# Kernel tuning notes

Hardware: AMD Instinct MI355X
Metric: run time of the kernel (lower is better)

Reference implementation:

```python
import jax, jax.numpy as jnp
import numpy as np

T_PRED = 30   # max_pred_time * hz
B = 2048      # number of trajectory segments (batch)
D = 256       # n_hidden_after_deconv
DH = 128      # n_hidden_after_deconv / 2


def setup_inputs() -> dict:
    key = jax.random.key(0)
    k1, k2, k3, k4 = jax.random.split(key, 4)
    return {
        "encode_samples": jax.random.normal(k1, (T_PRED, B, D), dtype=jnp.float32),
        "representation_cur": jax.random.normal(k2, (B, DH), dtype=jnp.float32),
        "Wk_w": jax.random.normal(k3, (T_PRED, D, DH), dtype=jnp.float32) * (1.0 / np.sqrt(DH)),
        "Wk_b": jax.random.normal(k4, (T_PRED, D), dtype=jnp.float32) * 0.01,
    }


def reference(encode_samples, representation_cur, Wk_w, Wk_b):
    # encode_samples: [T, B, D] future encoder outputs (c_{t+i})
    # Wk_w: [T, D, DH] per-step Linear weights (torch layout [out,in]); Wk_b: [T, D]
    T, Bn, Dd = encode_samples.shape
    # pred[i] = Wk[i](representation_cur)  -> [T, B, D]
    pred = jnp.einsum('bh,tdh->tbd', representation_cur, Wk_w) + Wk_b[:, None, :]
    # total_i = encode_samples[i] @ pred[i].T  -> [T, B, B]
    totals = jnp.einsum('tbd,tcd->tbc', encode_samples, pred)
    # nce += sum(diag(log_softmax(total, dim=1))) per step (torch LogSoftmax default dim=1 on 2D)
    logp = jax.nn.log_softmax(totals, axis=2)
    nce = jnp.sum(jnp.diagonal(logp, axis1=1, axis2=2))
    calc_step = Bn * T  # all pred_steps > T-1 (all segments long enough)
    nce = nce / (-1.0 * calc_step)
    # accuracy from the LAST step (matches the original loop-carried `correct`/`batch_idx`)
    probs = jax.nn.softmax(totals[-1], axis=1)          # softmax over dim=1
    correct = jnp.sum(jnp.argmax(probs, axis=0) == jnp.arange(Bn))  # argmax over dim=0
    accuracy = correct.astype(jnp.float32) / Bn
    return (accuracy, nce, jnp.asarray(Bn), jnp.asarray(calc_step))
```

## Files before the change

kernel.cpp:

```cpp
#include <hip/hip_runtime.h>
#include <math.h>

typedef unsigned short u16;
typedef unsigned int   u32;
typedef unsigned long long u64;

#define T_PRED 30
#define BN 2048
#define DD 256
#define DHH 128
#define ESHIFT 64.0f

typedef __attribute__((ext_vector_type(8))) short short8;
typedef __attribute__((ext_vector_type(4))) float f32x4;

#define WS_S      4096
#define WS_TABLE  (WS_S + 245760)
#define WS_ZEND   (WS_TABLE + 16384)
#define WS_WH     WS_ZEND
#define WS_WL     (WS_WH + 1966080)
#define WS_RH     (WS_WL + 1966080)
#define WS_RL     (WS_RH + 524288)
#define WS_GH     (WS_RL + 524288)
#define WS_GL29   (WS_GH + 15728640)
#define WS_T29    (WS_GL29 + 524288)

__device__ __forceinline__ u16 bf16_rne(float f) {
    u32 u = __float_as_uint(f);
    u32 r = u + 0x7fffu + ((u >> 16) & 1u);
    return (u16)(r >> 16);
}

__device__ __forceinline__ short8 pack_hi8(const float* f) {
    short8 r;
#pragma unroll
    for (int k = 0; k < 8; ++k) r[k] = (short)(u16)(__float_as_uint(f[k]) >> 16);
    return r;
}
__device__ __forceinline__ short8 pack_lo8(const float* f) {
    short8 r;
#pragma unroll
    for (int k = 0; k < 8; ++k) {
        float hf = __uint_as_float(__float_as_uint(f[k]) & 0xffff0000u);
        r[k] = (short)bf16_rne(f[k] - hf);
    }
    return r;
}

#define AS1 __attribute__((address_space(1)))
#define AS3 __attribute__((address_space(3)))

__global__ __launch_bounds__(256) void prep_kernel(
    const float* __restrict__ rep, const float* __restrict__ Ww,
    u16* __restrict__ Rh, u16* __restrict__ Rl,
    u16* __restrict__ Wh, u16* __restrict__ Wl, u32* __restrict__ wsz)
{
    const int bx = blockIdx.x, tid = threadIdx.x;
    for (int i = bx * 256 + tid; i < 66560; i += 32768) wsz[i] = 0;

    if (bx < 120) {
        __shared__ float tile[64][132];
        const int t = bx >> 2, d0 = (bx & 3) * 64;
        for (int it = 0; it < 8; ++it) {
            int idx = tid + it * 256;
            int row = idx >> 5, off = (idx & 31) * 4;
            *(float4*)&tile[row][off] =
                *(const float4*)&Ww[((size_t)t * DD + d0 + row) * DHH + off];
        }
        __syncthreads();
        const int h = tid >> 1, half = tid & 1;
        const bool lo = (t == T_PRED - 1);
        for (int d4 = 0; d4 < 32; d4 += 4) {
            ushort4 hv, lv;
            u16* hp = (u16*)&hv; u16* lp = (u16*)&lv;
#pragma unroll
            for (int k = 0; k < 4; ++k) {
                float v = tile[half * 32 + d4 + k][h];
                u16 hb = bf16_rne(v);
                hp[k] = hb;
                float hf = __uint_as_float((u32)hb << 16);
                lp[k] = bf16_rne(v - hf);
            }
            size_t o = (size_t)t * DHH * DD + (size_t)h * DD + d0 + half * 32 + d4;
            *(ushort4*)&Wh[o] = hv;
            if (lo) *(ushort4*)&Wl[o] = lv;
        }
    } else {
        int base = (bx - 120) * 256 + tid;
        for (int p = 0; p < 32; ++p) {
            int i = base + p * 2048;
            float4 v = ((const float4*)rep)[i];
            float vv[4] = {v.x, v.y, v.z, v.w};
            u16 h[4], l[4];
#pragma unroll
            for (int k = 0; k < 4; ++k) {
                h[k] = bf16_rne(vv[k]);
                float hf = __uint_as_float((u32)h[k] << 16);
                l[k] = bf16_rne(vv[k] - hf);
            }
            ((ushort4*)Rh)[i] = make_ushort4(h[0], h[1], h[2], h[3]);
            ((ushort4*)Rl)[i] = make_ushort4(l[0], l[1], l[2], l[3]);
        }
    }
}

__global__ __launch_bounds__(256) void g_fused_kernel(
    const float* __restrict__ E, const u16* __restrict__ Wh,
    const u16* __restrict__ Wl, u16* __restrict__ Gh,
    u16* __restrict__ Gh29, u16* __restrict__ Gl29)
{
    __shared__ __attribute__((aligned(16))) u32 esm[2][4096];
    __shared__ __attribute__((aligned(16))) u16 wsm[2][4096];
    const int y    = blockIdx.y;
    const int tid  = threadIdx.x;
    const int lane = tid & 63;
    const int w    = tid >> 6;
    const int ml   = lane & 15;
    const int quad = lane >> 4;

    if (y < 29) {
        const int t    = y;
        const int row0 = blockIdx.x * 128;
        const int wr   = (w >> 1) * 64;
        const int wc   = (w & 1) * 64;
        const float* Et = E + (size_t)t * BN * DD;
        const u16*   Wt = Wh + (size_t)t * DHH * DD;
        const int erow_l = lane >> 3, eunit = lane & 7;
        const int wcol_l = lane >> 2, wunit = lane & 3;

        auto stage = [&](int buf, int kc) {
#pragma unroll
            for (int n = 0; n < 4; ++n) {
                int q = w * 4 + n;
                int row = q * 8 + erow_l;
                int unit = (eunit - row) & 7;
                const float* g = Et + (size_t)(row0 + row) * DD + kc * 32 + unit * 4;
                __builtin_amdgcn_global_load_lds((const AS1 u32*)g,
                    (AS3 u32*)(&esm[buf][q * 256]), 16, 0, 0);
            }
#pragma unroll
            for (int n = 0; n < 2; ++n) {
                int q = w * 2 + n;
                int col = q * 16 + wcol_l;
                int unit = (wunit - col) & 3;
                const u16* g = Wt + (size_t)col * DD + kc * 32 + unit * 8;
                __builtin_amdgcn_global_load_lds((const AS1 u32*)g,
                    (AS3 u32*)(&wsm[buf][q * 512]), 16, 0, 0);
            }
        };

        f32x4 acc[4][4];
#pragma unroll
        for (int i = 0; i < 4; ++i)
#pragma unroll
            for (int j = 0; j < 4; ++j) acc[i][j] = (f32x4){0.f, 0.f, 0.f, 0.f};

        stage(0, 0);
        __syncthreads();
#pragma unroll 1
        for (int kc = 0; kc < 8; ++kc) {
            if (kc < 7) stage((kc + 1) & 1, kc + 1);
            const int pb = kc & 1;
            short8 ah[4], bh[4];
#pragma unroll
            for (int i = 0; i < 4; ++i) {
                int row = wr + i * 16 + ml;
                float4 f0 = *(const float4*)&esm[pb][row * 32 + (((quad * 2 + 0 + row) & 7) * 4)];
                float4 f1 = *(const float4*)&esm[pb][row * 32 + (((quad * 2 + 1 + row) & 7) * 4)];
                float f[8] = {f0.x, f0.y, f0.z, f0.w, f1.x, f1.y, f1.z, f1.w};
                ah[i] = pack_hi8(f);
            }
#pragma unroll
            for (int j = 0; j < 4; ++j) {
                int col = wc + j * 16 + ml;
                bh[j] = *(const short8*)&wsm[pb][col * 32 + ((quad + col) & 3) * 8];
            }
#pragma unroll
            for (int i = 0; i < 4; ++i)
#pragma unroll
                for (int j = 0; j < 4; ++j)
                    acc[i][j] = __builtin_amdgcn_mfma_f32_16x16x32_bf16(ah[i], bh[j], acc[i][j], 0, 0, 0);
            __syncthreads();
        }

#pragma unroll
        for (int i = 0; i < 4; ++i)
#pragma unroll
            for (int j = 0; j < 4; ++j)
#pragma unroll
                for (int r = 0; r < 4; ++r) {
                    int row = row0 + wr + i * 16 + quad * 4 + r;
                    int col = wc + j * 16 + ml;
                    Gh[((size_t)t * BN + row) * DHH + col] = bf16_rne(acc[i][j][r]);
                }
    } else {
        const int row0 = ((y - 29) * 16 + blockIdx.x) * 32;
        const int wc   = w * 32;
        const size_t tE = (size_t)(T_PRED - 1) * BN * DD;
        const size_t tW = (size_t)(T_PRED - 1) * DHH * DD;

#pragma unroll 1
        for (int rr = 0; rr < 32; rr += 16) {
            f32x4 acc[2];
            acc[0] = (f32x4){0.f, 0.f, 0.f, 0.f};
            acc[1] = (f32x4){0.f, 0.f, 0.f, 0.f};
#pragma unroll
            for (int kc = 0; kc < 8; ++kc) {
                const float* ep = E + tE + (size_t)(row0 + rr + ml) * DD + kc * 32 + quad * 8;
                float4 e0 = *(const float4*)ep;
                float4 e1 = *(const float4*)(ep + 4);
                float f[8] = {e0.x, e0.y, e0.z, e0.w, e1.x, e1.y, e1.z, e1.w};
                short8 ah = pack_hi8(f);
                short8 al = pack_lo8(f);
#pragma unroll
                for (int j = 0; j < 2; ++j) {
                    size_t o = tW + (size_t)(wc + j * 16 + ml) * DD + kc * 32 + quad * 8;
                    short8 bh = *(const short8*)(Wh + o);
                    short8 bl = *(const short8*)(Wl + o);
                    acc[j] = __builtin_amdgcn_mfma_f32_16x16x32_bf16(ah, bh, acc[j], 0, 0, 0);
                    acc[j] = __builtin_amdgcn_mfma_f32_16x16x32_bf16(ah, bl, acc[j], 0, 0, 0);
                    acc[j] = __builtin_amdgcn_mfma_f32_16x16x32_bf16(al, bh, acc[j], 0, 0, 0);
                }
            }
#pragma unroll
            for (int j = 0; j < 2; ++j)
#pragma unroll
                for (int r = 0; r < 4; ++r) {
                    int row = row0 + rr + quad * 4 + r;
                    int col = wc + j * 16 + ml;
                    float v = acc[j][r];
                    u16 hb = bf16_rne(v);
                    float hf = __uint_as_float((u32)hb << 16);
                    Gh29[(size_t)row * DHH + col] = hb;
                    Gl29[(size_t)row * DHH + col] = bf16_rne(v - hf);
                }
        }
    }
}

__global__ __launch_bounds__(128) void nce_fused_kernel(
    const u16* __restrict__ Gh, const u16* __restrict__ Gh29,
    const u16* __restrict__ Gl29, const u16* __restrict__ Rh,
    const u16* __restrict__ Rl, float* __restrict__ S,
    float* __restrict__ tot29, float* __restrict__ nce_acc)
{
    __shared__ __attribute__((aligned(16))) u16 sm[16384];
    const int z    = blockIdx.z;
    const int tid  = threadIdx.x;
    const int lane = tid & 63;
    const int w    = tid >> 6;
    const int ml   = lane & 15;
    const int quad = lane >> 4;
    float* S29 = S + (size_t)(T_PRED - 1) * BN;

    if (z < 29) {
        const int t      = z;
        const int row0   = blockIdx.x * 128;
        const int cq     = blockIdx.y;
        const int cchunk = cq * 512;
        const int wr     = w * 64;
        const bool dblk  = ((int)(blockIdx.x >> 2) == cq);
        const int scol_l = lane >> 4, sunit = lane & 15;

        auto stage = [&](int buf, int c0) {
#pragma unroll
            for (int n = 0; n < 8; ++n) {
                int q = w * 8 + n;
                int col = q * 4 + scol_l;
                int unit = (sunit - col) & 15;
                const u16* g = Rh + (size_t)(c0 + col) * DHH + unit * 8;
                __builtin_amdgcn_global_load_lds((const AS1 u32*)g,
                    (AS3 u32*)(&sm[buf * 8192 + q * 512]), 16, 0, 0);
            }
        };

        stage(0, cchunk);

        short8 ah[4][4];
#pragma unroll
        for (int i = 0; i < 4; ++i)
#pragma unroll
            for (int kc = 0; kc < 4; ++kc)
                ah[i][kc] = *(const short8*)(Gh +
                    ((size_t)t * BN + row0 + wr + i * 16 + ml) * DHH + kc * 32 + quad * 8);

        float ssum[4][4];
#pragma unroll
        for (int i = 0; i < 4; ++i)
#pragma unroll
            for (int r = 0; r < 4; ++r) ssum[i][r] = 0.f;
        float dsum = 0.f;

        __syncthreads();
#pragma unroll 1
        for (int it = 0; it < 8; ++it) {
            const int c0 = cchunk + it * 64;
            if (it < 7) stage((it + 1) & 1, c0 + 64);
            const int pb = it & 1;

            f32x4 acc[4][4];
#pragma unroll
            for (int i = 0; i < 4; ++i)
#pragma unroll
                for (int j = 0; j < 4; ++j) acc[i][j] = (f32x4){0.f, 0.f, 0.f, 0.f};

#pragma unroll
            for (int kc = 0; kc < 4; ++kc) {
                short8 bh[4];
#pragma unroll
                for (int j = 0; j < 4; ++j) {
                    int col = j * 16 + ml;
                    bh[j] = *(const short8*)&sm[pb * 8192 + col * 128
                              + (((kc << 2) + quad + col) & 15) * 8];
                }
#pragma unroll
                for (int i = 0; i < 4; ++i)
#pragma unroll
                    for (int j = 0; j < 4; ++j)
                        acc[i][j] = __builtin_amdgcn_mfma_f32_16x16x32_bf16(ah[i][kc], bh[j], acc[i][j], 0, 0, 0);
            }

            if (dblk && c0 == row0 + wr) {
#pragma unroll
                for (int i = 0; i < 4; ++i)
#pragma unroll
                    for (int j = 0; j < 4; ++j)
#pragma unroll
                        for (int r = 0; r < 4; ++r)
                            if (j * 16 + ml == i * 16 + quad * 4 + r)
                                dsum += acc[i][j][r];
            }
#pragma unroll
            for (int i = 0; i < 4; ++i)
#pragma unroll
                for (int r = 0; r < 4; ++r)
                    ssum[i][r] += __expf(acc[i][0][r] - ESHIFT)
                                + __expf(acc[i][1][r] - ESHIFT)
                                + __expf(acc[i][2][r] - ESHIFT)
                                + __expf(acc[i][3][r] - ESHIFT);
            __syncthreads();
        }

#pragma unroll
        for (int i = 0; i < 4; ++i)
#pragma unroll
            for (int r = 0; r < 4; ++r) {
                float v = ssum[i][r];
#pragma unroll
                for (int o = 1; o < 16; o <<= 1) v += __shfl_xor(v, o, 64);
                if (ml == 0)
                    atomicAdd(S + (size_t)t * BN + row0 + wr + i * 16 + quad * 4 + r, v);
            }
        if (dblk) {
            float dv = dsum;
#pragma unroll
            for (int o = 1; o < 64; o <<= 1) dv += __shfl_xor(dv, o, 64);
            if (lane == 0) atomicAdd(nce_acc, -dv);
        }
    } else {
        const int zz   = z - T_PRED + 1;
        const int row0 = (zz * 2 + (blockIdx.y >> 1)) * 64;
        const int col0 = (((int)blockIdx.x << 1) | (blockIdx.y & 1)) * 64;
        const bool dblk = (row0 == col0);

#pragma unroll
        for (int n = 0; n < 16; ++n) {
            int q = w * 16 + n;
            int half = q >> 4, qq = q & 15;
            int col = qq * 4 + (lane >> 4);
            int unit = ((lane & 15) - col) & 15;
            const u16* g = (half ? Rl : Rh) + (size_t)(col0 + col) * DHH + unit * 8;
            __builtin_amdgcn_global_load_lds((const AS1 u32*)g,
                (AS3 u32*)(&sm[q * 512]), 16, 0, 0);
        }

        short8 ah[2][4], al[2][4];
#pragma unroll
        for (int i = 0; i < 2; ++i)
#pragma unroll
            for (int kc = 0; kc < 4; ++kc) {
                size_t o = (size_t)(row0 + w * 32 + i * 16 + ml) * DHH + kc * 32 + quad * 8;
                ah[i][kc] = *(const short8*)(Gh29 + o);
                al[i][kc] = *(const short8*)(Gl29 + o);
            }

        f32x4 acc[2][4];
#pragma unroll
        for (int i = 0; i < 2; ++i)
#pragma unroll
            for (int j = 0; j < 4; ++j) acc[i][j] = (f32x4){0.f, 0.f, 0.f, 0.f};

        __syncthreads();
#pragma unroll
        for (int kc = 0; kc < 4; ++kc) {
            short8 bh[4], bl[4];
#pragma unroll
            for (int j = 0; j < 4; ++j) {
                int col = j * 16 + ml;
                int sl = (((kc << 2) + quad + col) & 15) * 8;
                bh[j] = *(const short8*)&sm[col * 128 + sl];
                bl[j] = *(const short8*)&sm[8192 + col * 128 + sl];
            }
#pragma unroll
            for (int i = 0; i < 2; ++i)
#pragma unroll
                for (int j = 0; j < 4; ++j) {
                    acc[i][j] = __builtin_amdgcn_mfma_f32_16x16x32_bf16(ah[i][kc], bh[j], acc[i][j], 0, 0, 0);
                    acc[i][j] = __builtin_amdgcn_mfma_f32_16x16x32_bf16(ah[i][kc], bl[j], acc[i][j], 0, 0, 0);
                    acc[i][j] = __builtin_amdgcn_mfma_f32_16x16x32_bf16(al[i][kc], bh[j], acc[i][j], 0, 0, 0);
                }
        }

        float dsum = 0.f;
#pragma unroll
        for (int i = 0; i < 2; ++i) {
#pragma unroll
            for (int r = 0; r < 4; ++r) {
                int row = row0 + w * 32 + i * 16 + quad * 4 + r;
                float es = 0.f;
#pragma unroll
                for (int j = 0; j < 4; ++j) {
                    int col = col0 + j * 16 + ml;
                    float v = acc[i][j][r];
                    tot29[(size_t)row * BN + col] = v;
                    es += __expf(v - ESHIFT);
                    if (dblk && col == row) dsum += v;
                }
#pragma unroll
                for (int o = 1; o < 16; o <<= 1) es += __shfl_xor(es, o, 64);
                if (ml == 0) atomicAdd(S29 + row, es);
            }
        }
        if (dblk) {
#pragma unroll
            for (int o = 1; o < 64; o <<= 1) dsum += __shfl_xor(dsum, o, 64);
            if (lane == 0) atomicAdd(nce_acc, -dsum);
        }
    }
}

__device__ __forceinline__ u32 fenc(float f) {
    u32 u = __float_as_uint(f);
    return (u & 0x80000000u) ? ~u : (u | 0x80000000u);
}

__global__ __launch_bounds__(256) void argmax_fin_kernel(
    const float* __restrict__ tot29, const float* __restrict__ S,
    u64* __restrict__ table, u32* __restrict__ done,
    float* __restrict__ nce_acc, float* __restrict__ out)
{
    __shared__ float lse_s[128];
    __shared__ float part[4];
    __shared__ u32 lastflag;
    __shared__ int cpart[4];
    const int tid = threadIdx.x;
    const int c   = blockIdx.x * 256 + tid;
    const int b0  = blockIdx.y * 128;
    const float* S29 = S + (size_t)(T_PRED - 1) * BN;

    {
        const int base = ((int)blockIdx.y * 8 + (int)blockIdx.x) * 480;
        float v = 0.f;
        for (int i = tid; i < 480; i += 256)
            v += ESHIFT + __logf(S[base + i]);
#pragma unroll
        for (int o = 1; o < 64; o <<= 1) v += __shfl_xor(v, o, 64);
        if ((tid & 63) == 0) part[tid >> 6] = v;
        __syncthreads();
        if (tid == 0)
            atomicAdd(nce_acc, part[0] + part[1] + part[2] + part[3]);
    }

    if (tid < 128) lse_s[tid] = ESHIFT + __logf(S29[b0 + tid]);
    __syncthreads();

    float best = -3.4e38f; int bi = 0;
    for (int b = 0; b < 128; ++b) {
        float v = tot29[(size_t)(b0 + b) * BN + c] - lse_s[b];
        if (v > best) { best = v; bi = b0 + b; }
    }
    u64 key = ((u64)fenc(best) << 32) | (u32)(0xFFFFFFFFu - (u32)bi);
    atomicMax(table + c, key);

    __threadfence();
    if (tid == 0) lastflag = (atomicAdd(done, 1u) == 127u);
    __syncthreads();
    if (!lastflag) return;

    int cnt = 0;
    for (int i = tid; i < BN; i += 256) {
        u64 k = atomicAdd(table + i, 0ull);
        u32 b = 0xFFFFFFFFu - (u32)(k & 0xFFFFFFFFull);
        if ((int)b == i) cnt++;
    }
#pragma unroll
    for (int o = 1; o < 64; o <<= 1) cnt += __shfl_xor(cnt, o, 64);
    if ((tid & 63) == 0) cpart[tid >> 6] = cnt;
    __syncthreads();
    if (tid == 0) {
        int correct = cpart[0] + cpart[1] + cpart[2] + cpart[3];
        float nce = atomicAdd(nce_acc, 0.0f);
        out[0] = (float)correct / (float)BN;
        out[1] = nce / (float)(BN * T_PRED);
        out[2] = (float)BN;
        out[3] = (float)(BN * T_PRED);
    }
}

extern "C" void kernel_launch(void* const* d_in, const int* in_sizes, int n_in,
                              void* d_out, int out_size, void* d_ws, size_t ws_size,
                              hipStream_t stream) {
    const float* E   = (const float*)d_in[0];
    const float* rep = (const float*)d_in[1];
    const float* Ww  = (const float*)d_in[2];
    float* out = (float*)d_out;

    char* ws = (char*)d_ws;
    float* nce_acc = (float*)(ws + 0);
    u32*   done    = (u32*)(ws + 8);
    float* S       = (float*)(ws + WS_S);
    u64*   table   = (u64*)(ws + WS_TABLE);
    u16*   Wh      = (u16*)(ws + WS_WH);
    u16*   Wl      = (u16*)(ws + WS_WL);
    u16*   Rh      = (u16*)(ws + WS_RH);
    u16*   Rl      = (u16*)(ws + WS_RL);
    u16*   Gh      = (u16*)(ws + WS_GH);
    u16*   Gh29    = Gh + (size_t)(T_PRED - 1) * BN * DHH;
    u16*   Gl29    = (u16*)(ws + WS_GL29);
    float* tot29   = (float*)(ws + WS_T29);

    prep_kernel<<<dim3(128), 256, 0, stream>>>(rep, Ww, Rh, Rl, Wh, Wl, (u32*)ws);
    g_fused_kernel<<<dim3(16, 33), 256, 0, stream>>>(E, Wh, Wl, Gh, Gh29, Gl29);
    nce_fused_kernel<<<dim3(16, 4, 45), 128, 0, stream>>>(Gh, Gh29, Gl29, Rh, Rl,
                                                          S, tot29, nce_acc);
    argmax_fin_kernel<<<dim3(8, 16), 256, 0, stream>>>(tot29, S, table, done,
                                                       nce_acc, out);
}
```

Before: 210.9 us.

## Retile NCE kernel into 256x256 blocks of 512 threads with full-tile LDS staging

The main NCE kernel now uses 512-thread blocks that each cover a 256-row by 256-column tile of a time step. The whole 256-column slice of R is staged into LDS once, replacing the double-buffered 64-column pipeline, and each wave computes a 32-row strip in 32-column chunks. The last-step split-precision path is remapped to 128x128 tiles with 16 rows per wave. Blocks drop from 2880 to 2112, which is meant to improve reuse of the staged B operand and cut per-block overhead. In exchange it doubles LDS use, gives up load/compute overlap inside a block, and lowers occupancy per CU.

```diff
diff --git a/kernel.cpp b/kernel.cpp
--- a/kernel.cpp
+++ b/kernel.cpp
@@ -238,13 +238,13 @@
     }
 }
 
-__global__ __launch_bounds__(128) void nce_fused_kernel(
+__global__ __launch_bounds__(512, 4) void nce_fused_kernel(
     const u16* __restrict__ Gh, const u16* __restrict__ Gh29,
     const u16* __restrict__ Gl29, const u16* __restrict__ Rh,
     const u16* __restrict__ Rl, float* __restrict__ S,
     float* __restrict__ tot29, float* __restrict__ nce_acc)
 {
-    __shared__ __attribute__((aligned(16))) u16 sm[16384];
+    __shared__ __attribute__((aligned(16))) u16 sm[32768];
     const int z    = blockIdx.z;
     const int tid  = threadIdx.x;
     const int lane = tid & 63;
@@ -254,102 +254,85 @@
     float* S29 = S + (size_t)(T_PRED - 1) * BN;
 
     if (z < 29) {
-        const int t      = z;
-        const int row0   = blockIdx.x * 128;
-        const int cq     = blockIdx.y;
-        const int cchunk = cq * 512;
-        const int wr     = w * 64;
-        const bool dblk  = ((int)(blockIdx.x >> 2) == cq);
-        const int scol_l = lane >> 4, sunit = lane & 15;
-
-        auto stage = [&](int buf, int c0) {
-#pragma unroll
-            for (int n = 0; n < 8; ++n) {
-                int q = w * 8 + n;
-                int col = q * 4 + scol_l;
-                int unit = (sunit - col) & 15;
-                const u16* g = Rh + (size_t)(c0 + col) * DHH + unit * 8;
-                __builtin_amdgcn_global_load_lds((const AS1 u32*)g,
-                    (AS3 u32*)(&sm[buf * 8192 + q * 512]), 16, 0, 0);
-            }
-        };
-
-        stage(0, cchunk);
-
-        short8 ah[4][4];
-#pragma unroll
-        for (int i = 0; i < 4; ++i)
+        const int t  = z;
+        const int c0 = (int)blockIdx.x << 8;
+        const int r0 = (int)blockIdx.y << 8;
+
+#pragma unroll
+        for (int n = 0; n < 8; ++n) {
+            const int q   = (w << 3) + n;
+            const int U   = (q << 6) | lane;
+            const int col = U >> 4;
+            const int g   = ((U & 15) - col) & 15;
+            const u16* src = Rh + (size_t)(c0 + col) * DHH + g * 8;
+            __builtin_amdgcn_global_load_lds((const AS1 u32*)src,
+                (AS3 u32*)(&sm[q << 9]), 16, 0, 0);
+        }
+
+        short8 ah[2][4];
+#pragma unroll
+        for (int i = 0; i < 2; ++i)
 #pragma unroll
             for (int kc = 0; kc < 4; ++kc)
                 ah[i][kc] = *(const short8*)(Gh +
-                    ((size_t)t * BN + row0 + wr + i * 16 + ml) * DHH + kc * 32 + quad * 8);
-
-        float ssum[4][4];
-#pragma unroll
-        for (int i = 0; i < 4; ++i)
+                    ((size_t)t * BN + r0 + (w << 5) + (i << 4) + ml) * DHH
+                    + (kc << 5) + (quad << 3));
+
+        float ssum[2][4];
+#pragma unroll
+        for (int i = 0; i < 2; ++i)
 #pragma unroll
             for (int r = 0; r < 4; ++r) ssum[i][r] = 0.f;
         float dsum = 0.f;
+        const bool dblk = (c0 == r0);
+        const int rbase = r0 + (w << 5) + (quad << 2);
 
         __syncthreads();
+
 #pragma unroll 1
-        for (int it = 0; it < 8; ++it) {
-            const int c0 = cchunk + it * 64;
-            if (it < 7) stage((it + 1) & 1, c0 + 64);
-            const int pb = it & 1;
-
-            f32x4 acc[4][4];
-#pragma unroll
-            for (int i = 0; i < 4; ++i)
-#pragma unroll
-                for (int j = 0; j < 4; ++j) acc[i][j] = (f32x4){0.f, 0.f, 0.f, 0.f};
+        for (int ch = 0; ch < 8; ++ch) {
+            f32x4 acc[2][2];
+#pragma unroll
+            for (int i = 0; i < 2; ++i)
+#pragma unroll
+                for (int j = 0; j < 2; ++j) acc[i][j] = (f32x4){0.f, 0.f, 0.f, 0.f};
 
 #pragma unroll
             for (int kc = 0; kc < 4; ++kc) {
-                short8 bh[4];
-#pragma unroll
-                for (int j = 0; j < 4; ++j) {
-                    int col = j * 16 + ml;
-                    bh[j] = *(const short8*)&sm[pb * 8192 + col * 128
-                              + (((kc << 2) + quad + col) & 15) * 8];
-                }
-#pragma unroll
-                for (int i = 0; i < 4; ++i)
-#pragma unroll
-                    for (int j = 0; j < 4; ++j)
-                        acc[i][j] = __builtin_amdgcn_mfma_f32_16x16x32_bf16(ah[i][kc], bh[j], acc[i][j], 0, 0, 0);
-            }
-
-            if (dblk && c0 == row0 + wr) {
-#pragma unroll
-                for (int i = 0; i < 4; ++i)
-#pragma unroll
-                    for (int j = 0; j < 4; ++j)
-#pragma unroll
-                        for (int r = 0; r < 4; ++r)
-                            if (j * 16 + ml == i * 16 + quad * 4 + r)
-                                dsum += acc[i][j][r];
-            }
-#pragma unroll
-            for (int i = 0; i < 4; ++i)
-#pragma unroll
-                for (int r = 0; r < 4; ++r)
-                    ssum[i][r] += __expf(acc[i][0][r] - ESHIFT)
-                                + __expf(acc[i][1][r] - ESHIFT)
-                                + __expf(acc[i][2][r] - ESHIFT)
-                                + __expf(acc[i][3][r] - ESHIFT);
-            __syncthreads();
-        }
-
-#pragma unroll
-        for (int i = 0; i < 4; ++i)
+                const int slot = ((kc << 2) + quad + ml) & 15;
+                const short8 bh0 = *(const short8*)&sm[((ch << 5) + ml) * 128 + (slot << 3)];
+                const short8 bh1 = *(const short8*)&sm[((ch << 5) + 16 + ml) * 128 + (slot << 3)];
+                acc[0][0] = __builtin_amdgcn_mfma_f32_16x16x32_bf16(ah[0][kc], bh0, acc[0][0], 0, 0, 0);
+                acc[0][1] = __builtin_amdgcn_mfma_f32_16x16x32_bf16(ah[0][kc], bh1, acc[0][1], 0, 0, 0);
+                acc[1][0] = __builtin_amdgcn_mfma_f32_16x16x32_bf16(ah[1][kc], bh0, acc[1][0], 0, 0, 0);
+                acc[1][1] = __builtin_amdgcn_mfma_f32_16x16x32_bf16(ah[1][kc], bh1, acc[1][1], 0, 0, 0);
+            }
+
+#pragma unroll
+            for (int i = 0; i < 2; ++i)
+#pragma unroll
+                for (int j = 0; j < 2; ++j)
+#pragma unroll
+                    for (int r = 0; r < 4; ++r) {
+                        float v = acc[i][j][r];
+                        ssum[i][r] += __expf(v - ESHIFT);
+                        if (dblk) {
+                            int row = rbase + (i << 4) + r;
+                            int col = c0 + (ch << 5) + (j << 4) + ml;
+                            if (row == col) dsum += v;
+                        }
+                    }
+        }
+
+#pragma unroll
+        for (int i = 0; i < 2; ++i)
 #pragma unroll
             for (int r = 0; r < 4; ++r) {
                 float v = ssum[i][r];
 #pragma unroll
                 for (int o = 1; o < 16; o <<= 1) v += __shfl_xor(v, o, 64);
                 if (ml == 0)
-                    atomicAdd(S + (size_t)t * BN + row0 + wr + i * 16 + quad * 4 + r, v);
+                    atomicAdd(S + (size_t)t * BN + rbase + (i << 4) + r, v);
             }
         if (dblk) {
             float dv = dsum;
@@ -358,83 +341,86 @@
             if (lane == 0) atomicAdd(nce_acc, -dv);
         }
     } else {
-        const int zz   = z - T_PRED + 1;
-        const int row0 = (zz * 2 + (blockIdx.y >> 1)) * 64;
-        const int col0 = (((int)blockIdx.x << 1) | (blockIdx.y & 1)) * 64;
-        const bool dblk = (row0 == col0);
-
-#pragma unroll
-        for (int n = 0; n < 16; ++n) {
-            int q = w * 16 + n;
-            int half = q >> 4, qq = q & 15;
-            int col = qq * 4 + (lane >> 4);
-            int unit = ((lane & 15) - col) & 15;
-            const u16* g = (half ? Rl : Rh) + (size_t)(col0 + col) * DHH + unit * 8;
-            __builtin_amdgcn_global_load_lds((const AS1 u32*)g,
-                (AS3 u32*)(&sm[q * 512]), 16, 0, 0);
-        }
-
-        short8 ah[2][4], al[2][4];
-#pragma unroll
-        for (int i = 0; i < 2; ++i)
+        const int idx = ((z - 29) << 6) + ((int)blockIdx.y << 3) + (int)blockIdx.x;
+        const int rb  = idx >> 4, cb = idx & 15;
+        const int r0  = rb << 7, c0 = cb << 7;
+        const bool dblk = (rb == cb);
+
+#pragma unroll
+        for (int n = 0; n < 8; ++n) {
+            const int q    = (w << 3) + n;
+            const int U    = (q << 6) | lane;
+            const int colL = (U >> 4) & 127;
+            const int half = U >> 11;
+            const int g    = ((U & 15) - colL) & 15;
+            const u16* src = (half ? Rl : Rh) + (size_t)(c0 + colL) * DHH + g * 8;
+            __builtin_amdgcn_global_load_lds((const AS1 u32*)src,
+                (AS3 u32*)(&sm[q << 9]), 16, 0, 0);
+        }
+
+        short8 ah[4], al[4];
+#pragma unroll
+        for (int kc = 0; kc < 4; ++kc) {
+            size_t o = (size_t)(r0 + (w << 4) + ml) * DHH + (kc << 5) + (quad << 3);
+            ah[kc] = *(const short8*)(Gh29 + o);
+            al[kc] = *(const short8*)(Gl29 + o);
+        }
+
+        float esum[4];
+#pragma unroll
+        for (int r = 0; r < 4; ++r) esum[r] = 0.f;
+        float dsum = 0.f;
+        const int rbase = r0 + (w << 4) + (quad << 2);
+
+        __syncthreads();
+
+#pragma unroll 1
+        for (int ch = 0; ch < 4; ++ch) {
+            f32x4 acc[2];
+            acc[0] = (f32x4){0.f, 0.f, 0.f, 0.f};
+            acc[1] = (f32x4){0.f, 0.f, 0.f, 0.f};
 #pragma unroll
             for (int kc = 0; kc < 4; ++kc) {
-                size_t o = (size_t)(row0 + w * 32 + i * 16 + ml) * DHH + kc * 32 + quad * 8;
-                ah[i][kc] = *(const short8*)(Gh29 + o);
-                al[i][kc] = *(const short8*)(Gl29 + o);
-            }
-
-        f32x4 acc[2][4];
-#pragma unroll
-        for (int i = 0; i < 2; ++i)
-#pragma unroll
-            for (int j = 0; j < 4; ++j) acc[i][j] = (f32x4){0.f, 0.f, 0.f, 0.f};
-
-        __syncthreads();
-#pragma unroll
-        for (int kc = 0; kc < 4; ++kc) {
-            short8 bh[4], bl[4];
-#pragma unroll
-            for (int j = 0; j < 4; ++j) {
-                int col = j * 16 + ml;
-                int sl = (((kc << 2) + quad + col) & 15) * 8;
-                bh[j] = *(const short8*)&sm[col * 128 + sl];
-                bl[j] = *(const short8*)&sm[8192 + col * 128 + sl];
-            }
-#pragma unroll
-            for (int i = 0; i < 2; ++i)
-#pragma unroll
-                for (int j = 0; j < 4; ++j) {
-                    acc[i][j] = __builtin_amdgcn_mfma_f32_16x16x32_bf16(ah[i][kc], bh[j], acc[i][j], 0, 0, 0);
-                    acc[i][j] = __builtin_amdgcn_mfma_f32_16x16x32_bf16(ah[i][kc], bl[j], acc[i][j], 0, 0, 0);
-                    acc[i][j] = __builtin_amdgcn_mfma_f32_16x16x32_bf16(al[i][kc], bh[j], acc[i][j], 0, 0, 0);
+                const int slot = ((kc << 2) + quad + ml) & 15;
+                const int i0 = ((ch << 5) + ml) * 128 + (slot << 3);
+                const int i1 = i0 + 16 * 128;
+                const short8 bh0 = *(const short8*)&sm[i0];
+                const short8 bl0 = *(const short8*)&sm[16384 + i0];
+                const short8 bh1 = *(const short8*)&sm[i1];
+                const short8 bl1 = *(const short8*)&sm[16384 + i1];
+                acc[0] = __builtin_amdgcn_mfma_f32_16x16x32_bf16(ah[kc], bh0, acc[0], 0, 0, 0);
+                acc[0] = __builtin_amdgcn_mfma_f32_16x16x32_bf16(ah[kc], bl0, acc[0], 0, 0, 0);
+                acc[0] = __builtin_amdgcn_mfma_f32_16x16x32_bf16(al[kc], bh0, acc[0], 0, 0, 0);
+                acc[1] = __builtin_amdgcn_mfma_f32_16x16x32_bf16(ah[kc], bh1, acc[1], 0, 0, 0);
+                acc[1] = __builtin_amdgcn_mfma_f32_16x16x32_bf16(ah[kc], bl1, acc[1], 0, 0, 0);
+                acc[1] = __builtin_amdgcn_mfma_f32_16x16x32_bf16(al[kc], bh1, acc[1], 0, 0, 0);
+            }
+
+#pragma unroll
+            for (int j = 0; j < 2; ++j)
+#pragma unroll
+                for (int r = 0; r < 4; ++r) {
+                    float v = acc[j][r];
+                    int row = rbase + r;
+                    int col = c0 + (ch << 5) + (j << 4) + ml;
+                    tot29[(size_t)row * BN + col] = v;
+                    esum[r] += __expf(v - ESHIFT);
+                    if (dblk && row == col) dsum += v;
                 }
         }
 
-        float dsum = 0.f;
-#pragma unroll
-        for (int i = 0; i < 2; ++i) {
-#pragma unroll
-            for (int r = 0; r < 4; ++r) {
-                int row = row0 + w * 32 + i * 16 + quad * 4 + r;
-                float es = 0.f;
-#pragma unroll
-                for (int j = 0; j < 4; ++j) {
-                    int col = col0 + j * 16 + ml;
-                    float v = acc[i][j][r];
-                    tot29[(size_t)row * BN + col] = v;
-                    es += __expf(v - ESHIFT);
-                    if (dblk && col == row) dsum += v;
-                }
-#pragma unroll
-                for (int o = 1; o < 16; o <<= 1) es += __shfl_xor(es, o, 64);
-                if (ml == 0) atomicAdd(S29 + row, es);
-            }
+#pragma unroll
+        for (int r = 0; r < 4; ++r) {
+            float v = esum[r];
+#pragma unroll
+            for (int o = 1; o < 16; o <<= 1) v += __shfl_xor(v, o, 64);
+            if (ml == 0) atomicAdd(S29 + rbase + r, v);
         }
         if (dblk) {
-#pragma unroll
-            for (int o = 1; o < 64; o <<= 1) dsum += __shfl_xor(dsum, o, 64);
-            if (lane == 0) atomicAdd(nce_acc, -dsum);
+            float dv = dsum;
+#pragma unroll
+            for (int o = 1; o < 64; o <<= 1) dv += __shfl_xor(dv, o, 64);
+            if (lane == 0) atomicAdd(nce_acc, -dv);
         }
     }
 }
@@ -531,8 +517,8 @@
 
     prep_kernel<<<dim3(128), 256, 0, stream>>>(rep, Ww, Rh, Rl, Wh, Wl, (u32*)ws);
     g_fused_kernel<<<dim3(16, 33), 256, 0, stream>>>(E, Wh, Wl, Gh, Gh29, Gl29);
-    nce_fused_kernel<<<dim3(16, 4, 45), 128, 0, stream>>>(Gh, Gh29, Gl29, Rh, Rl,
-                                                          S, tot29, nce_acc);
+    nce_fused_kernel<<<dim3(8, 8, 33), 512, 0, stream>>>(Gh, Gh29, Gl29, Rh, Rl,
+                                                         S, tot29, nce_acc);
     argmax_fin_kernel<<<dim3(8, 16), 256, 0, stream>>>(tot29, S, table, done,
                                                        nce_acc, out);
 }
```

New measurement: 189.2 us. -10.3%, faster.
